# Kernel tuning notes

Hardware: AMD Instinct MI355X
Metric: run time of the kernel (lower is better)

The kernel has to match this reference:

```python
import jax, jax.numpy as jnp
import numpy as np

B = 16
NC = 80
K = 5 + NC
STRIDES = (8.0, 16.0, 32.0)
HWS = ((80, 80), (40, 40), (20, 20))
ANCHORS = (
    ((10, 13), (16, 30), (33, 23)),
    ((30, 61), (62, 45), (59, 119)),
    ((116, 90), (156, 198), (373, 326)),
)
SCORE_THRESH = 0.25
NMS_THRESH = 0.45
DET_PER_IMG = 300
MAX_NMS = 1024          # fixed candidate budget per image (JIT-static)
MAX_COORD = 4096.0      # class offset for batched (per-class) NMS


def setup_inputs() -> dict:
    key = jax.random.key(0)
    ks = jax.random.split(key, 3)
    inp = {}
    for i, ((h, w), anc) in enumerate(zip(HWS, ANCHORS)):
        inp[f"head{i}"] = jax.random.normal(ks[i], (B, 3, h, w, K), dtype=jnp.float32)
        ys, xs = jnp.meshgrid(jnp.arange(h, dtype=jnp.float32), jnp.arange(w, dtype=jnp.float32), indexing="ij")
        inp[f"grid{i}"] = jnp.broadcast_to(jnp.stack([xs, ys], -1)[None, None], (1, 3, h, w, 2))
        inp[f"shift{i}"] = jnp.asarray(anc, dtype=jnp.float32).reshape(1, 3, 1, 1, 2)
    return inp


def _decode_level(head, grid, shift, stride):
    # sigmoid + yolov5 box decode (det_utils.decode_single)
    h = jax.nn.sigmoid(head)
    xy = (h[..., :2] * 2.0 - 0.5 + grid) * stride
    wh = (h[..., 2:4] * 2.0) ** 2 * shift
    logits = jnp.concatenate([xy, wh, h[..., 4:]], axis=-1)
    return logits.reshape(head.shape[0], -1, K)  # [B, A*H*W, K]


def _iou_matrix(b):
    area = (b[:, 2] - b[:, 0]) * (b[:, 3] - b[:, 1])
    lt = jnp.maximum(b[:, None, :2], b[None, :, :2])
    rb = jnp.minimum(b[:, None, 2:], b[None, :, 2:])
    wh = jnp.clip(rb - lt, 0.0)
    inter = wh[..., 0] * wh[..., 1]
    return inter / (area[:, None] + area[None, :] - inter + 1e-7)


def _postprocess_one(boxes, scores):
    # boxes: [P,4] xyxy, scores: [P,NC] = cls * obj
    flat = scores.reshape(-1)
    flat = jnp.where(flat > SCORE_THRESH, flat, 0.0)  # score threshold
    top_s, top_i = jax.lax.top_k(flat, MAX_NMS)       # sorted desc (NMS order)
    anchor_idx = top_i // NC
    cls = top_i % NC
    b = boxes[anchor_idx]                              # [M,4]
    bb = b + (cls.astype(b.dtype) * MAX_COORD)[:, None]  # per-class offset == batched_nms
    iou = _iou_matrix(bb)
    idx = jnp.arange(MAX_NMS)

    def body(i, keep):
        sup = (iou[i] > NMS_THRESH) & keep[i] & (idx > i)
        return keep & ~sup

    keep = jax.lax.fori_loop(0, MAX_NMS, body, top_s > 0.0)
    kept_s = jnp.where(keep, top_s, 0.0)
    fs, fi = jax.lax.top_k(kept_s, DET_PER_IMG)
    fb = jnp.where(fs[:, None] > 0.0, b[fi], 0.0)
    fl = jnp.where(fs > 0.0, cls[fi], -1)
    return fb, fs, fl


def reference(head0, head1, head2, grid0, grid1, grid2, shift0, shift1, shift2):
    heads = (head0, head1, head2)
    grids = (grid0, grid1, grid2)
    shifts = (shift0, shift1, shift2)
    preds = jnp.concatenate(
        [_decode_level(h, g, s, st) for h, g, s, st in zip(heads, grids, shifts, STRIDES)],
        axis=1,
    )  # [B, P, K]
    cxcy, wh = preds[..., :2], preds[..., 2:4]
    boxes = jnp.concatenate([cxcy - wh * 0.5, cxcy + wh * 0.5], axis=-1)  # cxcywh -> xyxy
    scores = preds[..., 5:] * preds[..., 4:5]
    boxes_out, scores_out, labels_out = jax.vmap(_postprocess_one)(boxes, scores)
    return boxes_out, scores_out, labels_out
```

## Files before the change

kernel.cpp:

```cpp
#include <hip/hip_runtime.h>
#include <cstdint>

#define NB 16
#define NCL 80
#define KDIM 85
#define NA 25200
#define NBINS 256
#define CAP 2048
#define MAXN 1024
#define NDET 300
#define NSLAB 396
#define SLOTS 416

__device__ __constant__ float c_ancw[9] = {10.f,16.f,33.f, 30.f,62.f,59.f, 116.f,156.f,373.f};
__device__ __constant__ float c_anch[9] = {13.f,30.f,23.f, 61.f,45.f,119.f, 90.f,198.f,326.f};
__device__ __constant__ int   c_seg_a0[9]    = {0,6400,12800,19200,20800,22400,24000,24400,24800};
__device__ __constant__ int   c_seg_cells[9] = {6400,6400,6400,1600,1600,1600,400,400,400};
__device__ __constant__ int   c_seg_ww[9]    = {80,80,80,40,40,40,20,20,20};
__device__ __constant__ float c_seg_str[9]   = {8.f,8.f,8.f,16.f,16.f,16.f,32.f,32.f,32.f};
__device__ __constant__ int   c_seg_slab0[9] = {0,100,200,300,325,350,375,382,389};

__device__ __forceinline__ float sgm(float x) { return 1.0f / (1.0f + expf(-x)); }
__device__ __forceinline__ int binof(float s) {
  int b = (int)((s - 0.25f) * 341.33334f);
  return b < 0 ? 0 : (b > NBINS - 1 ? NBINS - 1 : b);
}

struct Loc { const float* base; };
__device__ __forceinline__ Loc locate(const float* h0, const float* h1, const float* h2,
                                      int img, int a) {
  Loc L; const float* hp; int cells, rel;
  if (a < 19200)      { hp=h0; cells=6400; rel=a;       }
  else if (a < 24000) { hp=h1; cells=1600; rel=a-19200; }
  else                { hp=h2; cells=400;  rel=a-24000; }
  int ai = rel / cells; int cell = rel - ai*cells;
  L.base = hp + (size_t)((img*3 + ai)*cells + cell) * KDIM;
  return L;
}

__global__ void __launch_bounds__(256) k_decode(const float* __restrict__ h0,
    const float* __restrict__ h1, const float* __restrict__ h2,
    float* __restrict__ boxes, float* __restrict__ sobjv, unsigned* __restrict__ hist) {
  __shared__ unsigned lh[NBINS];
  __shared__ float4 buf4[(64 * KDIM) / 4];
  float* buf = (float*)buf4;
  int tid = threadIdx.x, img = blockIdx.y;
  for (int i = tid; i < NBINS; i += 256) lh[i] = 0;
  __syncthreads();
  for (int sl = 0; sl < 4; ++sl) {
    int slab = blockIdx.x * 4 + sl;
    int sg = 0;
    #pragma unroll
    for (int k = 1; k < 9; ++k) sg += (slab >= c_seg_slab0[k]);
    int sloc  = slab - c_seg_slab0[sg];
    int cells = c_seg_cells[sg];
    int c0    = sloc * 64;
    int ncell = min(64, cells - c0);
    const float* hp = (sg < 3) ? h0 : (sg < 6 ? h1 : h2);
    int ai = sg - (sg / 3) * 3;
    const float* src = hp + (size_t)((img*3 + ai)*cells + c0) * KDIM;
    int nf4 = (ncell * KDIM) >> 2;
    __syncthreads();
    const float4* src4 = (const float4*)src;
    for (int i = tid; i < nf4; i += 256) buf4[i] = src4[i];
    __syncthreads();
    int anc = tid >> 2, sub = tid & 3;
    if (anc < ncell) {
      const float* rec = &buf[anc * KDIM];
      float so = sgm(rec[4]);
      int cell = c0 + anc;
      int a = c_seg_a0[sg] + cell;
      if (sub == 0) {
        int ww = c_seg_ww[sg];
        int y;
        if (ww == 80) y = cell / 80; else if (ww == 40) y = cell / 40; else y = cell / 20;
        int x = cell - y*ww;
        float sx=sgm(rec[0]), sy=sgm(rec[1]), sw=sgm(rec[2]), sh=sgm(rec[3]);
        float st = c_seg_str[sg];
        float cx = (sx*2.0f - 0.5f + (float)x) * st;
        float cy = (sy*2.0f - 0.5f + (float)y) * st;
        float tw = sw*2.0f, th = sh*2.0f;
        float wv = (tw*tw) * c_ancw[sg];
        float hv = (th*th) * c_anch[sg];
        ((float4*)boxes)[(size_t)img*NA + a] =
            make_float4(cx - wv*0.5f, cy - hv*0.5f, cx + wv*0.5f, cy + hv*0.5f);
        sobjv[(size_t)img*NA + a] = so;
      }
      if (so > 0.25f) {
        float q = 0.25f / so;
        float cth = logf(q / (1.0f - q)) - 0.05f;
        #pragma unroll 4
        for (int k = 0; k < 20; ++k) {
          float c = rec[5 + sub*20 + k];
          if (c > cth) {
            float s = sgm(c) * so;
            if (s > 0.25f) atomicAdd(&lh[binof(s)], 1u);
          }
        }
      }
    }
  }
  __syncthreads();
  unsigned* gh = hist + (size_t)img * NBINS;
  for (int i = tid; i < NBINS; i += 256) { unsigned v = lh[i]; if (v) atomicAdd(&gh[i], v); }
}

__global__ void __launch_bounds__(256) k_thresh(const unsigned* __restrict__ hist,
                                                int* __restrict__ tbin) {
  int img = blockIdx.x, t = threadIdx.x;
  __shared__ unsigned sc[256];
  unsigned s = hist[(size_t)img*NBINS + t];
  sc[t] = s; __syncthreads();
  for (int d = 1; d < 256; d <<= 1) {
    unsigned add = (t + d < 256) ? sc[t + d] : 0u;
    __syncthreads(); sc[t] += add; __syncthreads();
  }
  unsigned inc = sc[t];
  unsigned excl = inc - s;
  if (excl < MAXN && inc >= MAXN) tbin[img] = t;
  if (t == 0 && sc[0] < MAXN) tbin[img] = 0;
}

__global__ void __launch_bounds__(256) k_compact(const float* __restrict__ h0,
    const float* __restrict__ h1, const float* __restrict__ h2,
    const float* __restrict__ sobjv, const int* __restrict__ tbin,
    unsigned* __restrict__ ccnt, unsigned long long* __restrict__ cand) {
  __shared__ unsigned long long lbuf[CAP];
  __shared__ unsigned lcnt, gbase;
  int img = blockIdx.y, tid = threadIdx.x;
  if (tid == 0) lcnt = 0;
  __syncthreads();
  int a = blockIdx.x * 256 + tid;
  int lane = tid & 63;
  int T = tbin[img];
  float gthr = 0.25f + (float)(T - 1) * (0.75f / (float)NBINS);
  float so = 0.0f; bool pass = false;
  if (a < NA) { so = sobjv[(size_t)img*NA + a]; pass = so > gthr; }
  unsigned long long m = __ballot(pass);
  while (m) {
    int srcl = __builtin_ctzll(m); m &= m - 1;
    int aa   = __shfl(a, srcl);
    float sso = __shfl(so, srcl);
    Loc L = locate(h0, h1, h2, img, aa);
    for (int c = lane; c < NCL; c += 64) {
      float s = sgm(L.base[5 + c]) * sso;
      if (s > 0.25f && binof(s) >= T) {
        unsigned p = atomicAdd(&lcnt, 1u);
        if (p < CAP) {
          unsigned idx = (unsigned)(aa * NCL + c);
          lbuf[p] = ((unsigned long long)__float_as_uint(s) << 32) | (unsigned)(~idx);
        }
      }
    }
  }
  __syncthreads();
  unsigned n = min(lcnt, (unsigned)CAP);
  if (tid == 0) gbase = atomicAdd(&ccnt[img], n);
  __syncthreads();
  unsigned b = gbase;
  for (unsigned i = tid; i < n; i += 256) {
    unsigned p = b + i;
    if (p < CAP) cand[(size_t)img*CAP + p] = lbuf[i];
  }
}

__global__ void __launch_bounds__(1024) k_sort(const unsigned long long* __restrict__ cand,
    const unsigned* __restrict__ ccnt, const float* __restrict__ boxes,
    float* __restrict__ tsc, int* __restrict__ tcls, float* __restrict__ traw,
    float* __restrict__ tbb, float* __restrict__ tarea,
    unsigned long long* __restrict__ keepinit) {
  __shared__ unsigned long long key[CAP];
  int img = blockIdx.x, t = threadIdx.x;
  int n = (int)min(ccnt[img], (unsigned)CAP);
  const unsigned long long* cb = cand + (size_t)img*CAP;
  key[t]        = (t < n)        ? cb[t]        : 0ull;
  key[t + 1024] = (t + 1024 < n) ? cb[t + 1024] : 0ull;
  __syncthreads();
  for (int k = 2; k <= CAP; k <<= 1) {
    for (int j = k >> 1; j > 0; j >>= 1) {
      #pragma unroll
      for (int eo = 0; eo < 2; ++eo) {
        int e = t + eo*1024;
        int l = e ^ j;
        if (l > e) {
          unsigned long long va = key[e], vb = key[l];
          bool up = (e & k) == 0;
          if (up ? (va < vb) : (va > vb)) { key[e] = vb; key[l] = va; }
        }
      }
      __syncthreads();
    }
  }
  unsigned long long kk = key[t];
  float s = __uint_as_float((unsigned)(kk >> 32));
  unsigned idx = ~(unsigned)kk;
  float b0=0,b1=0,b2=0,b3=0, bb0=0,bb1=0,bb2=0,bb3=0, ar=0; int cls=0;
  if (s > 0.0f) {
    unsigned anc = idx / NCL; cls = (int)(idx - anc*NCL);
    const float4 bp = ((const float4*)boxes)[(size_t)img*NA + anc];
    b0=bp.x; b1=bp.y; b2=bp.z; b3=bp.w;
    float off = (float)cls * 4096.0f;
    bb0=b0+off; bb1=b1+off; bb2=b2+off; bb3=b3+off;
    ar = (bb2-bb0)*(bb3-bb1);
  }
  int o = img*MAXN + t;
  tsc[o] = s; tcls[o] = cls; tarea[o] = ar;
  ((float4*)traw)[o] = make_float4(b0,b1,b2,b3);
  ((float4*)tbb)[o]  = make_float4(bb0,bb1,bb2,bb3);
  unsigned long long ball = __ballot(s > 0.0f);
  if ((t & 63) == 0) keepinit[img*16 + (t >> 6)] = ball;
}

__global__ void __launch_bounds__(256) k_iou(const float* __restrict__ tbb,
    const float* __restrict__ tarea, unsigned long long* __restrict__ sup,
    unsigned long long* __restrict__ rnz) {
  __shared__ float jx1[MAXN], jy1[MAXN], jx2[MAXN], jy2[MAXN], jar[MAXN];
  __shared__ unsigned rowflag;
  int img = blockIdx.y, t = threadIdx.x;
  if (t == 0) rowflag = 0;
  const float4* bbb = (const float4*)(tbb + (size_t)img*MAXN*4);
  const float* aab = tarea + (size_t)img*MAXN;
  for (int i = t; i < MAXN; i += 256) {
    float4 v = bbb[i];
    jx1[i]=v.x; jy1[i]=v.y; jx2[i]=v.z; jy2[i]=v.w; jar[i]=aab[i];
  }
  __syncthreads();
  int il = t >> 4, c = t & 15;
  int i = blockIdx.x*16 + il;
  float x1=jx1[i], y1=jy1[i], x2=jx2[i], y2=jy2[i], ai=jar[i];
  unsigned long long bits = 0;
  for (int l = 0; l < 64; ++l) {
    int ll = (l + c) & 63;
    int j = c*64 + ll;
    if (j > i) {
      float ltx = fmaxf(x1, jx1[j]), lty = fmaxf(y1, jy1[j]);
      float rbx = fminf(x2, jx2[j]), rby = fminf(y2, jy2[j]);
      float w = fmaxf(rbx - ltx, 0.0f), h = fmaxf(rby - lty, 0.0f);
      float inter = w*h;
      float iou = inter / (ai + jar[j] - inter + 1e-7f);
      if (iou > 0.45f) bits |= (1ull << ll);
    }
  }
  sup[((size_t)img*MAXN + i)*16 + c] = bits;
  if (bits) atomicOr(&rowflag, 1u << il);
  __syncthreads();
  if (t == 0 && rowflag) {
    int i0 = blockIdx.x * 16;
    atomicOr(&rnz[img*16 + (i0 >> 6)], (unsigned long long)rowflag << (i0 & 63));
  }
}

__global__ void __launch_bounds__(256) k_nms(const unsigned long long* __restrict__ keepinit,
    const unsigned long long* __restrict__ rnz, const unsigned long long* __restrict__ sup,
    const float* __restrict__ tsc, const int* __restrict__ tcls,
    const float* __restrict__ traw, float* __restrict__ out) {
  __shared__ unsigned long long rows[SLOTS*16];
  __shared__ unsigned short slotof[MAXN];
  __shared__ unsigned short rowof[SLOTS];
  __shared__ int scanbuf[256];
  __shared__ int order[MAXN];
  __shared__ unsigned long long s_rnz[16], s_keep[16];
  int img = blockIdx.x, tid = threadIdx.x;
  if (tid < 16) { s_rnz[tid] = rnz[img*16 + tid]; s_keep[tid] = keepinit[img*16 + tid]; }
  __syncthreads();
  unsigned nib = (unsigned)((s_rnz[tid >> 4] >> ((tid & 15)*4)) & 0xFull);
  int cnt4 = __popc(nib);
  scanbuf[tid] = cnt4; __syncthreads();
  for (int d = 1; d < 256; d <<= 1) {
    int add = (tid >= d) ? scanbuf[tid - d] : 0;
    __syncthreads(); scanbuf[tid] += add; __syncthreads();
  }
  int p = scanbuf[tid] - cnt4;
  #pragma unroll
  for (int k = 0; k < 4; ++k) {
    int r = tid*4 + k;
    if ((nib >> k) & 1) {
      if (p < SLOTS) { slotof[r] = (unsigned short)p; rowof[p] = (unsigned short)r; }
      else slotof[r] = 0xFFFF;
      ++p;
    } else slotof[r] = 0xFFFF;
  }
  __syncthreads();
  int nstage = min(scanbuf[255], SLOTS);
  for (int k = tid; k < nstage*16; k += 256)
    rows[k] = sup[((size_t)img*MAXN + rowof[k >> 4])*16 + (k & 15)];
  __syncthreads();
  if (tid < 64) {
    int lane = tid;
    unsigned long long keep = (lane < 16) ? s_keep[lane] : 0ull;
    unsigned long long rem  = (lane < 16) ? (s_keep[lane] & s_rnz[lane]) : 0ull;
    while (true) {
      int candi = MAXN;
      if (lane < 16 && rem) candi = lane*64 + __builtin_ctzll(rem);
      #pragma unroll
      for (int o = 32; o; o >>= 1) candi = min(candi, __shfl_xor(candi, o));
      if (candi >= MAXN) break;
      int sl = slotof[candi];
      unsigned long long row = 0;
      if (lane < 16)
        row = (sl != 0xFFFF) ? rows[sl*16 + lane]
                             : sup[((size_t)img*MAXN + candi)*16 + lane];
      keep &= ~row; rem &= ~row;
      if (lane == (candi >> 6)) rem &= ~(1ull << (candi & 63));
    }
    int cnt = (lane < 16) ? __popcll(keep) : 0;
    int inc = cnt;
    for (int d = 1; d < 64; d <<= 1) { int y = __shfl_up(inc, d); if (lane >= d) inc += y; }
    int total = __shfl(inc, 63);
    int base = inc - cnt;
    if (lane < 16) {
      unsigned long long mm = keep; int q = base;
      while (mm) { int b = __builtin_ctzll(mm); mm &= mm - 1; order[q++] = lane*64 + b; }
    }
    for (int r = lane; r < NDET; r += 64) {
      float4 fb = make_float4(0,0,0,0); float fs = 0.0f; float fl = -1.0f;
      if (r < total) {
        int o = img*MAXN + order[r];
        fs = tsc[o];
        fb = ((const float4*)traw)[o];
        fl = (float)tcls[o];
      }
      int ob = img*NDET + r;
      ((float4*)out)[ob] = fb;
      out[(size_t)NB*NDET*4 + ob] = fs;
      out[(size_t)NB*NDET*5 + ob] = fl;
    }
  }
}

constexpr size_t AL(size_t x){ return (x + 255) & ~size_t(255); }
constexpr size_t OFF_HIST = 0;
constexpr size_t OFF_CNT  = AL(OFF_HIST + (size_t)NB*NBINS*4);
constexpr size_t OFF_RNZ  = AL(OFF_CNT  + (size_t)NB*4);
constexpr size_t OFF_ZEND = AL(OFF_RNZ  + (size_t)NB*16*8);
constexpr size_t OFF_TBIN = OFF_ZEND;
constexpr size_t OFF_BOX  = AL(OFF_TBIN + (size_t)NB*4);
constexpr size_t OFF_SOBJ = AL(OFF_BOX  + (size_t)NB*NA*4*4);
constexpr size_t OFF_CAND = AL(OFF_SOBJ + (size_t)NB*NA*4);
constexpr size_t OFF_TSC  = AL(OFF_CAND + (size_t)NB*CAP*8);
constexpr size_t OFF_TCLS = AL(OFF_TSC  + (size_t)NB*MAXN*4);
constexpr size_t OFF_TRAW = AL(OFF_TCLS + (size_t)NB*MAXN*4);
constexpr size_t OFF_TBB  = AL(OFF_TRAW + (size_t)NB*MAXN*16);
constexpr size_t OFF_TAR  = AL(OFF_TBB  + (size_t)NB*MAXN*16);
constexpr size_t OFF_KEEP = AL(OFF_TAR  + (size_t)NB*MAXN*4);
constexpr size_t OFF_SUP  = AL(OFF_KEEP + (size_t)NB*16*8);

extern "C" void kernel_launch(void* const* d_in, const int* in_sizes, int n_in,
                              void* d_out, int out_size, void* d_ws, size_t ws_size,
                              hipStream_t stream) {
  const float *h0=nullptr,*h1=nullptr,*h2=nullptr;
  for (int i = 0; i < n_in; ++i) {
    if      (in_sizes[i] == NB*3*80*80*KDIM) h0 = (const float*)d_in[i];
    else if (in_sizes[i] == NB*3*40*40*KDIM) h1 = (const float*)d_in[i];
    else if (in_sizes[i] == NB*3*20*20*KDIM) h2 = (const float*)d_in[i];
  }
  char* ws = (char*)d_ws;
  unsigned* hist = (unsigned*)(ws + OFF_HIST);
  unsigned* ccnt = (unsigned*)(ws + OFF_CNT);
  unsigned long long* rnz = (unsigned long long*)(ws + OFF_RNZ);
  int* tbin      = (int*)(ws + OFF_TBIN);
  float* boxes   = (float*)(ws + OFF_BOX);
  float* sobjv   = (float*)(ws + OFF_SOBJ);
  unsigned long long* cand = (unsigned long long*)(ws + OFF_CAND);
  float* tsc     = (float*)(ws + OFF_TSC);
  int* tcls      = (int*)(ws + OFF_TCLS);
  float* traw    = (float*)(ws + OFF_TRAW);
  float* tbb     = (float*)(ws + OFF_TBB);
  float* tarea   = (float*)(ws + OFF_TAR);
  unsigned long long* keepinit = (unsigned long long*)(ws + OFF_KEEP);
  unsigned long long* sup      = (unsigned long long*)(ws + OFF_SUP);

  hipMemsetAsync(ws, 0, OFF_ZEND, stream);

  dim3 gdec(NSLAB/4, NB);
  k_decode <<<gdec, 256, 0, stream>>>(h0, h1, h2, boxes, sobjv, hist);
  k_thresh <<<NB, 256, 0, stream>>>(hist, tbin);
  dim3 gcmp((NA + 255)/256, NB);
  k_compact<<<gcmp, 256, 0, stream>>>(h0, h1, h2, sobjv, tbin, ccnt, cand);
  k_sort   <<<NB, 1024, 0, stream>>>(cand, ccnt, boxes, tsc, tcls, traw, tbb, tarea, keepinit);
  dim3 giou(MAXN/16, NB);
  k_iou    <<<giou, 256, 0, stream>>>(tbb, tarea, sup, rnz);
  k_nms    <<<NB, 256, 0, stream>>>(keepinit, rnz, sup, tsc, tcls, traw, (float*)d_out);
}
```

Measured before the change: 290.9 us.

## Fuse threshold, compaction and sort into one per-image select kernel

The threshold-scan, candidate-compaction and bitonic-sort kernels are merged into a single 1024-thread block per image that writes candidates straight into shared memory. This removes two launches and the global candidate buffer with its counters. The score histogram floor moves from 0.25 to 0.5 with finer bins, so fewer class scores trigger shared-memory atomics. Decode now computes objectness and the class cutoff once per anchor and shares them through shared memory instead of recomputing them in four lanes. The trade-off is that compaction runs on only 16 blocks, which cuts parallelism for the anchor scan.

```diff
diff --git a/kernel.cpp b/kernel.cpp
--- a/kernel.cpp
+++ b/kernel.cpp
@@ -11,6 +11,8 @@
 #define NDET 300
 #define NSLAB 396
 #define SLOTS 416
+#define SFLOOR 0.5f
+#define SSCALE 640.0f
 
 __device__ __constant__ float c_ancw[9] = {10.f,16.f,33.f, 30.f,62.f,59.f, 116.f,156.f,373.f};
 __device__ __constant__ float c_anch[9] = {13.f,30.f,23.f, 61.f,45.f,119.f, 90.f,198.f,326.f};
@@ -22,7 +24,7 @@
 
 __device__ __forceinline__ float sgm(float x) { return 1.0f / (1.0f + expf(-x)); }
 __device__ __forceinline__ int binof(float s) {
-  int b = (int)((s - 0.25f) * 341.33334f);
+  int b = (int)((s - SFLOOR) * SSCALE);
   return b < 0 ? 0 : (b > NBINS - 1 ? NBINS - 1 : b);
 }
 
@@ -43,10 +45,10 @@
     float* __restrict__ boxes, float* __restrict__ sobjv, unsigned* __restrict__ hist) {
   __shared__ unsigned lh[NBINS];
   __shared__ float4 buf4[(64 * KDIM) / 4];
+  __shared__ float soA[64], cthA[64];
   float* buf = (float*)buf4;
   int tid = threadIdx.x, img = blockIdx.y;
   for (int i = tid; i < NBINS; i += 256) lh[i] = 0;
-  __syncthreads();
   for (int sl = 0; sl < 4; ++sl) {
     int slab = blockIdx.x * 4 + sl;
     int sg = 0;
@@ -65,36 +67,45 @@
     for (int i = tid; i < nf4; i += 256) buf4[i] = src4[i];
     __syncthreads();
     int anc = tid >> 2, sub = tid & 3;
-    if (anc < ncell) {
+    if (sub == 0 && anc < ncell) {
       const float* rec = &buf[anc * KDIM];
       float so = sgm(rec[4]);
       int cell = c0 + anc;
       int a = c_seg_a0[sg] + cell;
-      if (sub == 0) {
-        int ww = c_seg_ww[sg];
-        int y;
-        if (ww == 80) y = cell / 80; else if (ww == 40) y = cell / 40; else y = cell / 20;
-        int x = cell - y*ww;
-        float sx=sgm(rec[0]), sy=sgm(rec[1]), sw=sgm(rec[2]), sh=sgm(rec[3]);
-        float st = c_seg_str[sg];
-        float cx = (sx*2.0f - 0.5f + (float)x) * st;
-        float cy = (sy*2.0f - 0.5f + (float)y) * st;
-        float tw = sw*2.0f, th = sh*2.0f;
-        float wv = (tw*tw) * c_ancw[sg];
-        float hv = (th*th) * c_anch[sg];
-        ((float4*)boxes)[(size_t)img*NA + a] =
-            make_float4(cx - wv*0.5f, cy - hv*0.5f, cx + wv*0.5f, cy + hv*0.5f);
-        sobjv[(size_t)img*NA + a] = so;
-      }
-      if (so > 0.25f) {
-        float q = 0.25f / so;
-        float cth = logf(q / (1.0f - q)) - 0.05f;
+      int ww = c_seg_ww[sg];
+      int y;
+      if (ww == 80) y = cell / 80; else if (ww == 40) y = cell / 40; else y = cell / 20;
+      int x = cell - y*ww;
+      float sx=sgm(rec[0]), sy=sgm(rec[1]), sw=sgm(rec[2]), sh=sgm(rec[3]);
+      float st = c_seg_str[sg];
+      float cx = (sx*2.0f - 0.5f + (float)x) * st;
+      float cy = (sy*2.0f - 0.5f + (float)y) * st;
+      float tw = sw*2.0f, th = sh*2.0f;
+      float wv = (tw*tw) * c_ancw[sg];
+      float hv = (th*th) * c_anch[sg];
+      ((float4*)boxes)[(size_t)img*NA + a] =
+          make_float4(cx - wv*0.5f, cy - hv*0.5f, cx + wv*0.5f, cy + hv*0.5f);
+      sobjv[(size_t)img*NA + a] = so;
+      soA[anc] = so;
+      float cth = 1e30f;
+      if (so > SFLOOR) {
+        float q = SFLOOR / so;
+        cth = logf(q / (1.0f - q)) - 0.05f;
+      }
+      cthA[anc] = cth;
+    }
+    __syncthreads();
+    if (anc < ncell) {
+      float so = soA[anc];
+      if (so > SFLOOR) {
+        float cth = cthA[anc];
+        const float* rec = &buf[anc * KDIM];
         #pragma unroll 4
         for (int k = 0; k < 20; ++k) {
           float c = rec[5 + sub*20 + k];
           if (c > cth) {
             float s = sgm(c) * so;
-            if (s > 0.25f) atomicAdd(&lh[binof(s)], 1u);
+            if (s > SFLOOR) atomicAdd(&lh[binof(s)], 1u);
           }
         }
       }
@@ -105,82 +116,69 @@
   for (int i = tid; i < NBINS; i += 256) { unsigned v = lh[i]; if (v) atomicAdd(&gh[i], v); }
 }
 
-__global__ void __launch_bounds__(256) k_thresh(const unsigned* __restrict__ hist,
-                                                int* __restrict__ tbin) {
-  int img = blockIdx.x, t = threadIdx.x;
-  __shared__ unsigned sc[256];
-  unsigned s = hist[(size_t)img*NBINS + t];
-  sc[t] = s; __syncthreads();
-  for (int d = 1; d < 256; d <<= 1) {
-    unsigned add = (t + d < 256) ? sc[t + d] : 0u;
-    __syncthreads(); sc[t] += add; __syncthreads();
-  }
-  unsigned inc = sc[t];
-  unsigned excl = inc - s;
-  if (excl < MAXN && inc >= MAXN) tbin[img] = t;
-  if (t == 0 && sc[0] < MAXN) tbin[img] = 0;
-}
-
-__global__ void __launch_bounds__(256) k_compact(const float* __restrict__ h0,
+__global__ void __launch_bounds__(1024) k_select(const float* __restrict__ h0,
     const float* __restrict__ h1, const float* __restrict__ h2,
-    const float* __restrict__ sobjv, const int* __restrict__ tbin,
-    unsigned* __restrict__ ccnt, unsigned long long* __restrict__ cand) {
-  __shared__ unsigned long long lbuf[CAP];
-  __shared__ unsigned lcnt, gbase;
-  int img = blockIdx.y, tid = threadIdx.x;
-  if (tid == 0) lcnt = 0;
-  __syncthreads();
-  int a = blockIdx.x * 256 + tid;
-  int lane = tid & 63;
-  int T = tbin[img];
-  float gthr = 0.25f + (float)(T - 1) * (0.75f / (float)NBINS);
-  float so = 0.0f; bool pass = false;
-  if (a < NA) { so = sobjv[(size_t)img*NA + a]; pass = so > gthr; }
-  unsigned long long m = __ballot(pass);
-  while (m) {
-    int srcl = __builtin_ctzll(m); m &= m - 1;
-    int aa   = __shfl(a, srcl);
-    float sso = __shfl(so, srcl);
-    Loc L = locate(h0, h1, h2, img, aa);
-    for (int c = lane; c < NCL; c += 64) {
-      float s = sgm(L.base[5 + c]) * sso;
-      if (s > 0.25f && binof(s) >= T) {
-        unsigned p = atomicAdd(&lcnt, 1u);
-        if (p < CAP) {
-          unsigned idx = (unsigned)(aa * NCL + c);
-          lbuf[p] = ((unsigned long long)__float_as_uint(s) << 32) | (unsigned)(~idx);
-        }
-      }
-    }
-  }
-  __syncthreads();
-  unsigned n = min(lcnt, (unsigned)CAP);
-  if (tid == 0) gbase = atomicAdd(&ccnt[img], n);
-  __syncthreads();
-  unsigned b = gbase;
-  for (unsigned i = tid; i < n; i += 256) {
-    unsigned p = b + i;
-    if (p < CAP) cand[(size_t)img*CAP + p] = lbuf[i];
-  }
-}
-
-__global__ void __launch_bounds__(1024) k_sort(const unsigned long long* __restrict__ cand,
-    const unsigned* __restrict__ ccnt, const float* __restrict__ boxes,
+    const float* __restrict__ sobjv, const unsigned* __restrict__ hist,
+    const float* __restrict__ boxes,
     float* __restrict__ tsc, int* __restrict__ tcls, float* __restrict__ traw,
     float* __restrict__ tbb, float* __restrict__ tarea,
     unsigned long long* __restrict__ keepinit) {
   __shared__ unsigned long long key[CAP];
-  int img = blockIdx.x, t = threadIdx.x;
-  int n = (int)min(ccnt[img], (unsigned)CAP);
-  const unsigned long long* cb = cand + (size_t)img*CAP;
-  key[t]        = (t < n)        ? cb[t]        : 0ull;
-  key[t + 1024] = (t + 1024 < n) ? cb[t + 1024] : 0ull;
+  __shared__ unsigned sc[256];
+  __shared__ unsigned lcnt;
+  __shared__ int sT;
+  int img = blockIdx.x, tid = threadIdx.x;
+  unsigned s0 = 0;
+  if (tid < 256) { s0 = hist[(size_t)img*NBINS + tid]; sc[tid] = s0; }
+  if (tid == 0) lcnt = 0;
+  __syncthreads();
+  for (int d = 1; d < 256; d <<= 1) {
+    unsigned add = 0;
+    if (tid < 256 && tid + d < 256) add = sc[tid + d];
+    __syncthreads();
+    if (tid < 256) sc[tid] += add;
+    __syncthreads();
+  }
+  if (tid < 256) {
+    unsigned inc = sc[tid], excl = inc - s0;
+    if (excl < MAXN && inc >= MAXN) sT = tid;
+    if (tid == 0 && sc[0] < MAXN) sT = 0;
+  }
+  __syncthreads();
+  int T = sT;
+  float gthr = (T == 0) ? 0.25f : (SFLOOR + (float)(T - 1) * (1.0f / SSCALE));
+  int lane = tid & 63;
+  for (int it = 0; it < (NA + 1023) / 1024; ++it) {
+    int a = it * 1024 + tid;
+    float so = 0.0f; bool pass = false;
+    if (a < NA) { so = sobjv[(size_t)img*NA + a]; pass = so > gthr; }
+    unsigned long long m = __ballot(pass);
+    while (m) {
+      int srcl = __builtin_ctzll(m); m &= m - 1;
+      int aa   = __shfl(a, srcl);
+      float sso = __shfl(so, srcl);
+      Loc L = locate(h0, h1, h2, img, aa);
+      for (int c = lane; c < NCL; c += 64) {
+        float s = sgm(L.base[5 + c]) * sso;
+        if (s > 0.25f && binof(s) >= T) {
+          unsigned p = atomicAdd(&lcnt, 1u);
+          if (p < CAP) {
+            unsigned idx = (unsigned)(aa * NCL + c);
+            key[p] = ((unsigned long long)__float_as_uint(s) << 32) | (unsigned)(~idx);
+          }
+        }
+      }
+    }
+  }
+  __syncthreads();
+  unsigned n = min(lcnt, (unsigned)CAP);
+  for (unsigned i = tid; i < CAP; i += 1024) if (i >= n) key[i] = 0ull;
   __syncthreads();
   for (int k = 2; k <= CAP; k <<= 1) {
     for (int j = k >> 1; j > 0; j >>= 1) {
       #pragma unroll
       for (int eo = 0; eo < 2; ++eo) {
-        int e = t + eo*1024;
+        int e = tid + eo*1024;
         int l = e ^ j;
         if (l > e) {
           unsigned long long va = key[e], vb = key[l];
@@ -191,7 +189,7 @@
       __syncthreads();
     }
   }
-  unsigned long long kk = key[t];
+  unsigned long long kk = key[tid];
   float s = __uint_as_float((unsigned)(kk >> 32));
   unsigned idx = ~(unsigned)kk;
   float b0=0,b1=0,b2=0,b3=0, bb0=0,bb1=0,bb2=0,bb3=0, ar=0; int cls=0;
@@ -203,12 +201,12 @@
     bb0=b0+off; bb1=b1+off; bb2=b2+off; bb3=b3+off;
     ar = (bb2-bb0)*(bb3-bb1);
   }
-  int o = img*MAXN + t;
+  int o = img*MAXN + tid;
   tsc[o] = s; tcls[o] = cls; tarea[o] = ar;
   ((float4*)traw)[o] = make_float4(b0,b1,b2,b3);
   ((float4*)tbb)[o]  = make_float4(bb0,bb1,bb2,bb3);
   unsigned long long ball = __ballot(s > 0.0f);
-  if ((t & 63) == 0) keepinit[img*16 + (t >> 6)] = ball;
+  if ((tid & 63) == 0) keepinit[img*16 + (tid >> 6)] = ball;
 }
 
 __global__ void __launch_bounds__(256) k_iou(const float* __restrict__ tbb,
@@ -330,14 +328,11 @@
 
 constexpr size_t AL(size_t x){ return (x + 255) & ~size_t(255); }
 constexpr size_t OFF_HIST = 0;
-constexpr size_t OFF_CNT  = AL(OFF_HIST + (size_t)NB*NBINS*4);
-constexpr size_t OFF_RNZ  = AL(OFF_CNT  + (size_t)NB*4);
+constexpr size_t OFF_RNZ  = AL(OFF_HIST + (size_t)NB*NBINS*4);
 constexpr size_t OFF_ZEND = AL(OFF_RNZ  + (size_t)NB*16*8);
-constexpr size_t OFF_TBIN = OFF_ZEND;
-constexpr size_t OFF_BOX  = AL(OFF_TBIN + (size_t)NB*4);
+constexpr size_t OFF_BOX  = OFF_ZEND;
 constexpr size_t OFF_SOBJ = AL(OFF_BOX  + (size_t)NB*NA*4*4);
-constexpr size_t OFF_CAND = AL(OFF_SOBJ + (size_t)NB*NA*4);
-constexpr size_t OFF_TSC  = AL(OFF_CAND + (size_t)NB*CAP*8);
+constexpr size_t OFF_TSC  = AL(OFF_SOBJ + (size_t)NB*NA*4);
 constexpr size_t OFF_TCLS = AL(OFF_TSC  + (size_t)NB*MAXN*4);
 constexpr size_t OFF_TRAW = AL(OFF_TCLS + (size_t)NB*MAXN*4);
 constexpr size_t OFF_TBB  = AL(OFF_TRAW + (size_t)NB*MAXN*16);
@@ -356,12 +351,9 @@
   }
   char* ws = (char*)d_ws;
   unsigned* hist = (unsigned*)(ws + OFF_HIST);
-  unsigned* ccnt = (unsigned*)(ws + OFF_CNT);
   unsigned long long* rnz = (unsigned long long*)(ws + OFF_RNZ);
-  int* tbin      = (int*)(ws + OFF_TBIN);
   float* boxes   = (float*)(ws + OFF_BOX);
   float* sobjv   = (float*)(ws + OFF_SOBJ);
-  unsigned long long* cand = (unsigned long long*)(ws + OFF_CAND);
   float* tsc     = (float*)(ws + OFF_TSC);
   int* tcls      = (int*)(ws + OFF_TCLS);
   float* traw    = (float*)(ws + OFF_TRAW);
@@ -374,10 +366,8 @@
 
   dim3 gdec(NSLAB/4, NB);
   k_decode <<<gdec, 256, 0, stream>>>(h0, h1, h2, boxes, sobjv, hist);
-  k_thresh <<<NB, 256, 0, stream>>>(hist, tbin);
-  dim3 gcmp((NA + 255)/256, NB);
-  k_compact<<<gcmp, 256, 0, stream>>>(h0, h1, h2, sobjv, tbin, ccnt, cand);
-  k_sort   <<<NB, 1024, 0, stream>>>(cand, ccnt, boxes, tsc, tcls, traw, tbb, tarea, keepinit);
+  k_select <<<NB, 1024, 0, stream>>>(h0, h1, h2, sobjv, hist, boxes,
+                                     tsc, tcls, traw, tbb, tarea, keepinit);
   dim3 giou(MAXN/16, NB);
   k_iou    <<<giou, 256, 0, stream>>>(tbb, tarea, sup, rnz);
   k_nms    <<<NB, 256, 0, stream>>>(keepinit, rnz, sup, tsc, tcls, traw, (float*)d_out);
```

Result: slower. 418.8 us (+44.0%).
